# Kernel tuning notes

Measured on AMD Instinct MI355X. Metric: run time of the kernel, lower is better.

The kernel has to match this reference:

```python
import jax, jax.numpy as jnp
import numpy as np


def setup_inputs() -> dict:
    key = jax.random.key(0)
    k1, k2 = jax.random.split(key)
    B, H, W = 64, 1024, 1024
    output = jax.random.normal(k1, (B, H, W), dtype=jnp.float32)
    target = jax.random.normal(k2, (B, H, W), dtype=jnp.float32)
    return {"output": output, "target": target, "patch_size": 64}


def reference(output, target, patch_size):
    # output, target: [B, H, W]; tile into non-overlapping p x p patches,
    # per-patch mean |o - t|, max over patches per image, mean over batch.
    B, H, W = output.shape
    p = patch_size
    nh, nw = H // p, W // p
    diff = jnp.abs(output - target)                      # [B, H, W]
    # [B, nh, p, nw, p] -> per-patch mean over the two p axes
    patch_l1 = diff.reshape(B, nh, p, nw, p).mean(axis=(2, 4))  # [B, nh, nw]
    max_patch_loss = patch_l1.max(axis=(1, 2))           # [B]
    # original initializes max at 0; L1 >= 0 so max with 0 is a no-op, kept for fidelity
    max_patch_loss = jnp.maximum(max_patch_loss, 0.0)
    return max_patch_loss.mean()
```

## Files before the change

### kernel.cpp

```cpp
#include <hip/hip_runtime.h>

#define BATCH   64
#define HEIGHT  1024
#define WIDTH   1024
#define PSZ     64
#define NPH     16
#define NPW     16
#define NPATCH  (NPH * NPW)

__global__ __launch_bounds__(256) void patch_mean_abs_kernel(
    const float* __restrict__ out_p, const float* __restrict__ tgt_p,
    float* __restrict__ patch_l1)
{
    const int blk   = blockIdx.x;
    const int b     = blk >> 8;
    const int patch = blk & 255;
    const int ph    = patch >> 4;
    const int pw    = patch & 15;

    const size_t base = (size_t)b * (HEIGHT * (size_t)WIDTH)
                      + (size_t)ph * PSZ * WIDTH
                      + (size_t)pw * PSZ;

    const int tid = threadIdx.x;
    const int r0  = tid >> 4;
    const int c4  = (tid & 15) * 4;

    float s = 0.f;
#pragma unroll
    for (int rr = 0; rr < 4; ++rr) {
        const size_t off = base + (size_t)(r0 + rr * 16) * WIDTH + c4;
        const float4 o = *reinterpret_cast<const float4*>(out_p + off);
        const float4 t = *reinterpret_cast<const float4*>(tgt_p + off);
        s += fabsf(o.x - t.x) + fabsf(o.y - t.y)
           + fabsf(o.z - t.z) + fabsf(o.w - t.w);
    }

#pragma unroll
    for (int off = 32; off > 0; off >>= 1)
        s += __shfl_down(s, off, 64);

    __shared__ float lds[4];
    if ((tid & 63) == 0) lds[tid >> 6] = s;
    __syncthreads();
    if (tid == 0) {
        const float tot = lds[0] + lds[1] + lds[2] + lds[3];
        patch_l1[blk] = tot * (1.0f / (PSZ * PSZ));
    }
}

__global__ __launch_bounds__(256) void finalize_kernel(
    const float* __restrict__ patch_l1, float* __restrict__ result)
{
    __shared__ float lds[4];
    const int tid = threadIdx.x;
    float acc = 0.f;

    for (int img = 0; img < BATCH; ++img) {
        float v = patch_l1[img * NPATCH + tid];
#pragma unroll
        for (int off = 32; off > 0; off >>= 1)
            v = fmaxf(v, __shfl_down(v, off, 64));
        if ((tid & 63) == 0) lds[tid >> 6] = v;
        __syncthreads();
        if (tid == 0)
            acc += fmaxf(fmaxf(lds[0], lds[1]), fmaxf(lds[2], lds[3]));
        __syncthreads();
    }
    if (tid == 0) result[0] = acc * (1.0f / BATCH);
}

extern "C" void kernel_launch(void* const* d_in, const int* in_sizes, int n_in,
                              void* d_out, int out_size, void* d_ws, size_t ws_size,
                              hipStream_t stream) {
    const float* out_p = (const float*)d_in[0];
    const float* tgt_p = (const float*)d_in[1];
    float* patch_l1 = (float*)d_ws;
    float* result   = (float*)d_out;

    patch_mean_abs_kernel<<<BATCH * NPATCH, 256, 0, stream>>>(out_p, tgt_p, patch_l1);
    finalize_kernel<<<1, 256, 0, stream>>>(patch_l1, result);
}
```

Measured before the change: 533.9 us.

## Process full patch-row strips per block and fold the per-image max into it

Each block now handles a full 64-row strip of one image, reading contiguous full-width rows with float4 loads and reducing per-patch sums with 16-lane shuffles. The per-strip max over patches is taken in the first kernel. The finalize kernel becomes a single parallel max/sum pass instead of a serial loop over images. This aims to improve coalescing and cut block count and finalize latency, at the risk of lower occupancy with fewer, longer-running blocks.

```diff
diff --git a/kernel.cpp b/kernel.cpp
--- a/kernel.cpp
+++ b/kernel.cpp
@@ -6,68 +6,66 @@
 #define PSZ     64
 #define NPH     16
 #define NPW     16
-#define NPATCH  (NPH * NPW)
 
-__global__ __launch_bounds__(256) void patch_mean_abs_kernel(
+__global__ __launch_bounds__(256) void patch_rowstrip_kernel(
     const float* __restrict__ out_p, const float* __restrict__ tgt_p,
-    float* __restrict__ patch_l1)
+    float* __restrict__ blk_max)
 {
-    const int blk   = blockIdx.x;
-    const int b     = blk >> 8;
-    const int patch = blk & 255;
-    const int ph    = patch >> 4;
-    const int pw    = patch & 15;
+    const int blk  = blockIdx.x;
+    const int img  = blk >> 4;
+    const int prow = blk & 15;
 
-    const size_t base = (size_t)b * (HEIGHT * (size_t)WIDTH)
-                      + (size_t)ph * PSZ * WIDTH
-                      + (size_t)pw * PSZ;
+    const size_t base = (size_t)img * (HEIGHT * (size_t)WIDTH)
+                      + (size_t)prow * PSZ * WIDTH
+                      + (size_t)threadIdx.x * 4;
 
-    const int tid = threadIdx.x;
-    const int r0  = tid >> 4;
-    const int c4  = (tid & 15) * 4;
+    const float4* __restrict__ po = reinterpret_cast<const float4*>(out_p + base);
+    const float4* __restrict__ pt = reinterpret_cast<const float4*>(tgt_p + base);
+    const int row_stride_f4 = WIDTH / 4;
 
-    float s = 0.f;
-#pragma unroll
-    for (int rr = 0; rr < 4; ++rr) {
-        const size_t off = base + (size_t)(r0 + rr * 16) * WIDTH + c4;
-        const float4 o = *reinterpret_cast<const float4*>(out_p + off);
-        const float4 t = *reinterpret_cast<const float4*>(tgt_p + off);
-        s += fabsf(o.x - t.x) + fabsf(o.y - t.y)
-           + fabsf(o.z - t.z) + fabsf(o.w - t.w);
+    float s0 = 0.f, s1 = 0.f;
+#pragma unroll 8
+    for (int r = 0; r < PSZ; ++r) {
+        const float4 a = po[(size_t)r * row_stride_f4];
+        const float4 c = pt[(size_t)r * row_stride_f4];
+        s0 += fabsf(a.x - c.x) + fabsf(a.y - c.y);
+        s1 += fabsf(a.z - c.z) + fabsf(a.w - c.w);
     }
+    float s = s0 + s1;
 
 #pragma unroll
-    for (int off = 32; off > 0; off >>= 1)
-        s += __shfl_down(s, off, 64);
+    for (int off = 8; off > 0; off >>= 1)
+        s += __shfl_down(s, off, 16);
 
-    __shared__ float lds[4];
-    if ((tid & 63) == 0) lds[tid >> 6] = s;
+    __shared__ float lds[NPW];
+    if ((threadIdx.x & 15) == 0) lds[threadIdx.x >> 4] = s;
     __syncthreads();
-    if (tid == 0) {
-        const float tot = lds[0] + lds[1] + lds[2] + lds[3];
-        patch_l1[blk] = tot * (1.0f / (PSZ * PSZ));
+    if (threadIdx.x == 0) {
+        float m = lds[0];
+#pragma unroll
+        for (int i = 1; i < NPW; ++i) m = fmaxf(m, lds[i]);
+        blk_max[blk] = m * (1.0f / (PSZ * PSZ));
     }
 }
 
-__global__ __launch_bounds__(256) void finalize_kernel(
-    const float* __restrict__ patch_l1, float* __restrict__ result)
+__global__ __launch_bounds__(256) void final_reduce_kernel(
+    const float* __restrict__ blk_max, float* __restrict__ result)
 {
+    const int t = threadIdx.x;
+    const float4 v = reinterpret_cast<const float4*>(blk_max)[t];
+    float m = fmaxf(fmaxf(v.x, v.y), fmaxf(v.z, v.w));
+    m = fmaxf(m, __shfl_down(m, 2, 4));
+    m = fmaxf(m, __shfl_down(m, 1, 4));
+    float contrib = ((t & 3) == 0) ? m : 0.0f;
+#pragma unroll
+    for (int off = 32; off > 0; off >>= 1)
+        contrib += __shfl_down(contrib, off, 64);
+
     __shared__ float lds[4];
-    const int tid = threadIdx.x;
-    float acc = 0.f;
-
-    for (int img = 0; img < BATCH; ++img) {
-        float v = patch_l1[img * NPATCH + tid];
-#pragma unroll
-        for (int off = 32; off > 0; off >>= 1)
-            v = fmaxf(v, __shfl_down(v, off, 64));
-        if ((tid & 63) == 0) lds[tid >> 6] = v;
-        __syncthreads();
-        if (tid == 0)
-            acc += fmaxf(fmaxf(lds[0], lds[1]), fmaxf(lds[2], lds[3]));
-        __syncthreads();
-    }
-    if (tid == 0) result[0] = acc * (1.0f / BATCH);
+    if ((t & 63) == 0) lds[t >> 6] = contrib;
+    __syncthreads();
+    if (t == 0)
+        result[0] = (lds[0] + lds[1] + lds[2] + lds[3]) * (1.0f / BATCH);
 }
 
 extern "C" void kernel_launch(void* const* d_in, const int* in_sizes, int n_in,
@@ -75,9 +73,9 @@
                               hipStream_t stream) {
     const float* out_p = (const float*)d_in[0];
     const float* tgt_p = (const float*)d_in[1];
-    float* patch_l1 = (float*)d_ws;
-    float* result   = (float*)d_out;
+    float* blk_max = (float*)d_ws;
+    float* result  = (float*)d_out;
 
-    patch_mean_abs_kernel<<<BATCH * NPATCH, 256, 0, stream>>>(out_p, tgt_p, patch_l1);
-    finalize_kernel<<<1, 256, 0, stream>>>(patch_l1, result);
+    patch_rowstrip_kernel<<<BATCH * NPH, 256, 0, stream>>>(out_p, tgt_p, blk_max);
+    final_reduce_kernel<<<1, 256, 0, stream>>>(blk_max, result);
 }
```

After: 500.9 us. 1.07x faster.
